# Optimization experiments

Measured on AMD Instinct MI355X. Metric: run time of the kernel, lower is better.

Reference implementation:

```python
import jax, jax.numpy as jnp
import numpy as np

N_NODES = 50000
N_EDGES = 800000
N_GRAPHS = 64
IN_C = 64
HID = 64
HEADS = 4
NEG_SLOPE = 0.2
EPS = 1e-16


def setup_inputs() -> dict:
    key = jax.random.key(0)
    ks = jax.random.split(key, 16)
    x = jax.random.normal(ks[0], (N_NODES, IN_C), dtype=jnp.float32)
    edge_index = jax.random.randint(ks[1], (2, N_EDGES), 0, N_NODES, dtype=jnp.int64)
    batch = jnp.sort(jax.random.randint(ks[2], (N_NODES,), 0, N_GRAPHS, dtype=jnp.int64))
    s = 1.0 / np.sqrt(IN_C)
    s2 = 1.0 / np.sqrt(HID * HEADS)
    s3 = 1.0 / np.sqrt(HID)
    return {
        "x": x,
        "edge_index": edge_index,
        "batch": batch,
        # GATv2 layer 1: in 64 -> heads*64 = 256 (concat)
        "Wl1": jax.random.normal(ks[3], (IN_C, HEADS * HID), dtype=jnp.float32) * s,
        "Wr1": jax.random.normal(ks[4], (IN_C, HEADS * HID), dtype=jnp.float32) * s,
        "att1": jax.random.normal(ks[5], (HEADS, HID), dtype=jnp.float32) * s3,
        "b1": jnp.zeros((HEADS * HID,), dtype=jnp.float32),
        # GATv2 layer 2: in 256 -> 1 head * 64
        "Wl2": jax.random.normal(ks[6], (HEADS * HID, HID), dtype=jnp.float32) * s2,
        "Wr2": jax.random.normal(ks[7], (HEADS * HID, HID), dtype=jnp.float32) * s2,
        "att2": jax.random.normal(ks[8], (1, HID), dtype=jnp.float32) * s3,
        "b2": jnp.zeros((HID,), dtype=jnp.float32),
        # MLP head: 64 -> 64 -> 2
        "W3": jax.random.normal(ks[9], (HID, 64), dtype=jnp.float32) * s3,
        "b3": jnp.zeros((64,), dtype=jnp.float32),
        "W4": jax.random.normal(ks[10], (64, 2), dtype=jnp.float32) * (1.0 / 8.0),
        "b4": jnp.zeros((2,), dtype=jnp.float32),
    }


def gatv2_conv(x, src, dst, Wl, Wr, att, bias, heads, out_c, n_nodes):
    # PyG GATv2Conv (eval mode, add_self_loops=False, concat heads):
    # x_l = lin_l(x) used for SOURCE nodes (messages), x_r = lin_r(x) for TARGET nodes.
    xl = (x @ Wl).reshape(n_nodes, heads, out_c)
    xr = (x @ Wr).reshape(n_nodes, heads, out_c)
    e = jax.nn.leaky_relu(xl[src] + xr[dst], NEG_SLOPE)          # [E, H, C]
    logits = jnp.einsum('ehc,hc->eh', e, att)                    # [E, H]
    # numerically stable softmax over incoming edges of each target node
    m = jax.ops.segment_max(logits, dst, num_segments=n_nodes)   # [N, H]
    ex = jnp.exp(logits - m[dst])
    denom = jax.ops.segment_sum(ex, dst, num_segments=n_nodes)   # [N, H]
    alpha = ex / (denom[dst] + EPS)                              # [E, H]
    out = jax.ops.segment_sum(alpha[:, :, None] * xl[src], dst, num_segments=n_nodes)
    return out.reshape(n_nodes, heads * out_c) + bias


def reference(x, edge_index, batch, Wl1, Wr1, att1, b1, Wl2, Wr2, att2, b2, W3, b3, W4, b4):
    src, dst = edge_index[0], edge_index[1]
    n = x.shape[0]
    h = gatv2_conv(x, src, dst, Wl1, Wr1, att1, b1, HEADS, HID, n)
    h = jax.nn.elu(h)
    h = gatv2_conv(h, src, dst, Wl2, Wr2, att2, b2, 1, HID, n)
    h = jax.nn.elu(h)
    # global mean pool over graphs
    sums = jax.ops.segment_sum(h, batch, num_segments=N_GRAPHS)
    cnt = jax.ops.segment_sum(jnp.ones((n,), dtype=h.dtype), batch, num_segments=N_GRAPHS)
    pooled = sums / jnp.maximum(cnt, 1.0)[:, None]
    # MLP head (dropout inactive in eval)
    z = jax.nn.relu(pooled @ W3 + b3)
    return z @ W4 + b4
```

## Files before the change

### kernel.cpp

```cpp
#include <hip/hip_runtime.h>
#include <hip/hip_fp16.h>
#include <math.h>

#define N_NODES 50000
#define N_EDGES 800000
#define N_GRAPHS 64
#define L2E 1.44269504f

#if __has_builtin(__builtin_amdgcn_fdot2)
#define HAS_FDOT2 1
typedef _Float16 h2_t __attribute__((ext_vector_type(2)));
#else
#define HAS_FDOT2 0
#endif

typedef _Float16 f16x8 __attribute__((ext_vector_type(8)));
typedef float f32x4 __attribute__((ext_vector_type(4)));

__device__ __forceinline__ float elu1(float v){ return v > 0.f ? v : expm1f(v); }

__device__ __forceinline__ __half2 bcast_h2(float e){
    return __builtin_bit_cast(__half2, __builtin_amdgcn_cvt_pkrtz(e, e));
}

__device__ __forceinline__ float pkdot(float4 q, const __half2* r2,
        const __half2* A6, const __half2* A4){
    const __half2* qh = (const __half2*)&q;
    float p = 0.f;
#if HAS_FDOT2
    #pragma unroll
    for (int i=0;i<4;i++){
        __half2 u = __hadd2(qh[i], r2[i]);
        __half2 ua = __builtin_bit_cast(__half2,
            __builtin_bit_cast(unsigned, u) & 0x7FFF7FFFu);
        p = __builtin_amdgcn_fdot2(__builtin_bit_cast(h2_t,u),
                                   __builtin_bit_cast(h2_t,A6[i]), p, false);
        p = __builtin_amdgcn_fdot2(__builtin_bit_cast(h2_t,ua),
                                   __builtin_bit_cast(h2_t,A4[i]), p, false);
    }
#else
    #pragma unroll
    for (int i=0;i<4;i++){
        float2 qf = __half22float2(qh[i]);
        float2 rf = __half22float2(r2[i]);
        float2 s6 = __half22float2(A6[i]);
        float2 s4 = __half22float2(A4[i]);
        float u0 = qf.x + rf.x, u1 = qf.y + rf.y;
        p = fmaf(s6.x, u0, fmaf(s4.x, fabsf(u0), p));
        p = fmaf(s6.y, u1, fmaf(s4.y, fabsf(u1), p));
    }
#endif
    return p;
}

__global__ __launch_bounds__(256) void k_prep(const float* __restrict__ x,
        const float* __restrict__ Wl1, const float* __restrict__ Wr1,
        const float* __restrict__ Wl2, const float* __restrict__ Wr2,
        const int* __restrict__ ei,
        __half* __restrict__ xh, __half* __restrict__ Wt1, __half* __restrict__ Wt2,
        int* __restrict__ deg, int* __restrict__ ranks, float* __restrict__ pooled){
    int t = threadIdx.x, bk = blockIdx.x;
    if (bk < 782){
        int e4 = bk*256 + t;
        if (e4 < N_EDGES/4){
            int4 d = ((const int4*)(ei + N_EDGES))[e4];
            int4 r;
            r.x = atomicAdd(&deg[d.x],1);
            r.y = atomicAdd(&deg[d.y],1);
            r.z = atomicAdd(&deg[d.z],1);
            r.w = atomicAdd(&deg[d.w],1);
            ((int4*)ranks)[e4] = r;
        }
    } else if (bk < 3907){
        int idx = (bk-782)*256 + t;
        float4 v = ((const float4*)x)[idx];
        __half2* dst = (__half2*)xh + (size_t)idx*2;
        dst[0] = __floats2half2_rn(v.x, v.y);
        dst[1] = __floats2half2_rn(v.z, v.w);
    } else {
        int elem = (bk-3907)*256 + t;
        if (elem < 32768){
            int c = elem >> 6, k = elem & 63;
            float v = (c < 256) ? Wl1[k*256 + c] : Wr1[k*256 + (c-256)];
            Wt1[elem] = __float2half(v);
        } else {
            int e2 = elem - 32768;
            int c = e2 >> 8, k = e2 & 255;
            float v = (c < 64) ? Wl2[k*64 + c] : Wr2[k*64 + (c-64)];
            Wt2[e2] = __float2half(v);
        }
        if (elem < N_GRAPHS*64) pooled[elem] = 0.f;
    }
}

__global__ __launch_bounds__(1024) void k_scan_a(const int* __restrict__ deg,
        int* __restrict__ rowptr, int* __restrict__ partial){
    __shared__ int s[1024];
    int t = threadIdx.x; int i = blockIdx.x*1024 + t;
    int v = (i < N_NODES) ? deg[i] : 0;
    s[t] = v; __syncthreads();
    for (int off=1; off<1024; off<<=1){
        int add = (t>=off) ? s[t-off] : 0;
        __syncthreads();
        s[t] += add;
        __syncthreads();
    }
    if (i < N_NODES) rowptr[i] = s[t] - v;
    if (t == 1023) partial[blockIdx.x] = s[1023];
}

__global__ __launch_bounds__(1024) void k_scan_c(int* __restrict__ rowptr,
        const int* __restrict__ partial){
    __shared__ int base;
    if (threadIdx.x == 0){
        int run = 0;
        for (int bk=0; bk<(int)blockIdx.x; bk++) run += partial[bk];
        base = run;
    }
    __syncthreads();
    int i = blockIdx.x*1024 + threadIdx.x;
    if (i < N_NODES){
        rowptr[i] += base;
    } else if (i == N_NODES){
        rowptr[N_NODES] = N_EDGES;
    }
}

__global__ __launch_bounds__(256) void k_mm1(const __half* __restrict__ xh,
        const __half* __restrict__ Wt1,
        __half* __restrict__ xl1h, __half* __restrict__ xr1h,
        const int* __restrict__ ei, const int* __restrict__ ranks,
        const int* __restrict__ rowptr, int* __restrict__ srcs){
    if (blockIdx.y == 0){
        int e4 = blockIdx.x*256 + threadIdx.x;
        if (e4 < N_EDGES/4){
            int4 sv = ((const int4*)ei)[e4];
            int4 dv = ((const int4*)(ei + N_EDGES))[e4];
            int4 rv = ((const int4*)ranks)[e4];
            __builtin_nontemporal_store(sv.x, &srcs[rowptr[dv.x] + rv.x]);
            __builtin_nontemporal_store(sv.y, &srcs[rowptr[dv.y] + rv.y]);
            __builtin_nontemporal_store(sv.z, &srcs[rowptr[dv.z] + rv.z]);
            __builtin_nontemporal_store(sv.w, &srcs[rowptr[dv.w] + rv.w]);
        }
        return;
    }
    __shared__ __half lds[4][16*136];
    int w = threadIdx.x >> 6, l = threadIdx.x & 63;
    int r0 = blockIdx.x*64 + w*16;
    int lr = l & 15, lk = l >> 4, lk4 = lk*4;
    int ar = r0 + lr; if (ar >= N_NODES) ar = N_NODES-1;
    const __half* arow = xh + (size_t)ar*64;
    f16x8 a0 = *(const f16x8*)(arow + lk*8);
    f16x8 a1 = *(const f16x8*)(arow + 32 + lk*8);
    #pragma unroll
    for (int cg=0; cg<4; cg++){
        f32x4 acc[8];
        #pragma unroll
        for (int ct=0; ct<8; ct++) acc[ct] = (f32x4){0.f,0.f,0.f,0.f};
        #pragma unroll
        for (int ct=0; ct<8; ct++){
            int col = cg*128 + ct*16 + lr;
            const __half* brow = Wt1 + (size_t)col*64;
            f16x8 b0 = *(const f16x8*)(brow + lk*8);
            f16x8 b1 = *(const f16x8*)(brow + 32 + lk*8);
            acc[ct] = __builtin_amdgcn_mfma_f32_16x16x32_f16(a0, b0, acc[ct], 0,0,0);
            acc[ct] = __builtin_amdgcn_mfma_f32_16x16x32_f16(a1, b1, acc[ct], 0,0,0);
        }
        #pragma unroll
        for (int ct=0; ct<8; ct++){
            #pragma unroll
            for (int i=0;i<4;i++)
                lds[w][(lk4+i)*136 + ct*16 + lr] = __float2half(acc[ct][i]);
        }
        __half* base = (cg < 2) ? xl1h : xr1h;
        int cbase = (cg & 1)*128;
        #pragma unroll
        for (int rr=0; rr<4; rr++){
            int row = rr*4 + lk;
            float4 v = *(const float4*)&lds[w][row*136 + lr*8];
            int grow = r0 + row;
            if (grow < N_NODES)
                *(float4*)&base[(size_t)grow*256 + cbase + lr*8] = v;
        }
    }
}

__global__ __launch_bounds__(256) void k_mm2(const __half* __restrict__ h1h,
        const __half* __restrict__ Wt2,
        __half* __restrict__ xl2h, __half* __restrict__ xr2h){
    __shared__ __half lds[4][16*72];
    int w = threadIdx.x >> 6, l = threadIdx.x & 63;
    int r0 = blockIdx.x*64 + w*16;
    int lr = l & 15, lk = l >> 4, lk4 = lk*4;
    int ar = r0 + lr; if (ar >= N_NODES) ar = N_NODES-1;
    const __half* arow = h1h + (size_t)ar*256;
    f16x8 a[8];
    #pragma unroll
    for (int ks=0; ks<8; ks++) a[ks] = *(const f16x8*)(arow + ks*32 + lk*8);
    #pragma unroll
    for (int cg=0; cg<2; cg++){
        f32x4 acc[4];
        #pragma unroll
        for (int ct=0; ct<4; ct++) acc[ct] = (f32x4){0.f,0.f,0.f,0.f};
        #pragma unroll
        for (int ks=0; ks<8; ks++){
            #pragma unroll
            for (int ct=0; ct<4; ct++){
                int col = cg*64 + ct*16 + lr;
                f16x8 bf = *(const f16x8*)(Wt2 + (size_t)col*256 + ks*32 + lk*8);
                acc[ct] = __builtin_amdgcn_mfma_f32_16x16x32_f16(a[ks], bf, acc[ct], 0,0,0);
            }
        }
        #pragma unroll
        for (int ct=0; ct<4; ct++){
            #pragma unroll
            for (int i=0;i<4;i++)
                lds[w][(lk4+i)*72 + ct*16 + lr] = __float2half(acc[ct][i]);
        }
        __half* base = (cg == 0) ? xl2h : xr2h;
        #pragma unroll
        for (int rr=0; rr<2; rr++){
            int row = rr*8 + (l>>3);
            float4 v = *(const float4*)&lds[w][row*72 + (l&7)*8];
            int grow = r0 + row;
            if (grow < N_NODES)
                *(float4*)&base[(size_t)grow*64 + (l&7)*8] = v;
        }
    }
}

__global__ __launch_bounds__(256) void k_gat1(const __half* __restrict__ xlh,
        const __half* __restrict__ xrh, const int* __restrict__ srcs,
        const int* __restrict__ rowptr, const float* __restrict__ att,
        const float* __restrict__ b, __half* __restrict__ h1h){
    int w = threadIdx.x >> 6, l = threadIdx.x & 63;
    int n = blockIdx.x*4 + w;
    int g = l >> 5, sub = l & 31;
    const float4* xh4 = (const float4*)xlh;
    float4 rq = *(const float4*)(xrh + (size_t)n*256 + sub*8);
    __half2 r2[4];
    { const __half2* rh = (const __half2*)&rq;
      r2[0]=rh[0]; r2[1]=rh[1]; r2[2]=rh[2]; r2[3]=rh[3]; }
    float4 A0v = *(const float4*)(att + sub*8);
    float4 A1v = *(const float4*)(att + sub*8 + 4);
    const float C6 = 0.6f*L2E, C4 = 0.4f*L2E;
    __half2 A6[4] = { __floats2half2_rn(A0v.x*C6, A0v.y*C6),
                      __floats2half2_rn(A0v.z*C6, A0v.w*C6),
                      __floats2half2_rn(A1v.x*C6, A1v.y*C6),
                      __floats2half2_rn(A1v.z*C6, A1v.w*C6) };
    __half2 A4[4] = { __floats2half2_rn(A0v.x*C4, A0v.y*C4),
                      __floats2half2_rn(A0v.z*C4, A0v.w*C4),
                      __floats2half2_rn(A1v.x*C4, A1v.y*C4),
                      __floats2half2_rn(A1v.z*C4, A1v.w*C4) };
    const __half2 Z2 = __floats2half2_rn(0.f, 0.f);
    float accf[8];
    #pragma unroll
    for (int c=0;c<8;c++) accf[c]=0.f;
    float dacc = 0.f;
    int beg = rowptr[n], end = rowptr[n+1];

    auto body = [&](int j, bool checked){
        int j0=j+g, j1=j+2+g, j2=j+4+g, j3=j+6+g;
        bool c0=true, c1=true, c2=true, c3=true;
        if (checked){
            c0 = j0<end; c1 = j1<end; c2 = j2<end; c3 = j3<end;
            j0 = c0?j0:beg; j1 = c1?j1:beg; j2 = c2?j2:beg; j3 = c3?j3:beg;
        }
        int s0 = srcs[j0], s1 = srcs[j1], s2 = srcs[j2], s3 = srcs[j3];
        float4 q0 = xh4[(unsigned)(s0*32 + sub)];
        float4 q1 = xh4[(unsigned)(s1*32 + sub)];
        float4 q2 = xh4[(unsigned)(s2*32 + sub)];
        float4 q3 = xh4[(unsigned)(s3*32 + sub)];
        float p0 = pkdot(q0, r2, A6, A4);
        float p1 = pkdot(q1, r2, A6, A4);
        float p2 = pkdot(q2, r2, A6, A4);
        float p3 = pkdot(q3, r2, A6, A4);
        #pragma unroll
        for (int off=1; off<8; off<<=1){
            p0 += __shfl_xor(p0, off);
            p1 += __shfl_xor(p1, off);
            p2 += __shfl_xor(p2, off);
            p3 += __shfl_xor(p3, off);
        }
        float e0 = exp2f(p0), e1 = exp2f(p1), e2 = exp2f(p2), e3 = exp2f(p3);
        if (checked){
            e0 = c0?e0:0.f; e1 = c1?e1:0.f; e2 = c2?e2:0.f; e3 = c3?e3:0.f;
        }
        __half2 E0 = bcast_h2(e0);
        __half2 E1 = bcast_h2(e1);
        __half2 E2 = bcast_h2(e2);
        __half2 E3 = bcast_h2(e3);
        const __half2* q0h = (const __half2*)&q0;
        const __half2* q1h = (const __half2*)&q1;
        const __half2* q2h = (const __half2*)&q2;
        const __half2* q3h = (const __half2*)&q3;
        #pragma unroll
        for (int i=0;i<4;i++){
            __half2 a16 = __hfma2(E0, q0h[i], Z2);
            a16 = __hfma2(E1, q1h[i], a16);
            a16 = __hfma2(E2, q2h[i], a16);
            a16 = __hfma2(E3, q3h[i], a16);
            float2 f = __half22float2(a16);
            accf[2*i]   += f.x;
            accf[2*i+1] += f.y;
        }
        dacc += e0 + e1 + e2 + e3;
    };

    int j = beg;
    int nfull = (end - beg) >> 3;
    for (int it=0; it<nfull; ++it, j+=8) body(j, false);
    if (j < end) body(j, true);

    #pragma unroll
    for (int c=0;c<8;c++) accf[c] += __shfl_xor(accf[c], 32);
    dacc += __shfl_xor(dacc, 32);
    if (l < 32){
        float inv = 1.f / (dacc + 1e-16f);
        float4 B0 = *(const float4*)(b + l*8);
        float4 B1 = *(const float4*)(b + l*8 + 4);
        float4 st;
        __half2* sp = (__half2*)&st;
        sp[0] = __floats2half2_rn(elu1(fmaf(accf[0],inv,B0.x)), elu1(fmaf(accf[1],inv,B0.y)));
        sp[1] = __floats2half2_rn(elu1(fmaf(accf[2],inv,B0.z)), elu1(fmaf(accf[3],inv,B0.w)));
        sp[2] = __floats2half2_rn(elu1(fmaf(accf[4],inv,B1.x)), elu1(fmaf(accf[5],inv,B1.y)));
        sp[3] = __floats2half2_rn(elu1(fmaf(accf[6],inv,B1.z)), elu1(fmaf(accf[7],inv,B1.w)));
        *(float4*)(h1h + (size_t)n*256 + l*8) = st;
    }
}

__global__ __launch_bounds__(256) void k_gat2(const __half* __restrict__ xlh,
        const __half* __restrict__ xrh, const int* __restrict__ srcs,
        const int* __restrict__ rowptr, const float* __restrict__ att,
        const float* __restrict__ b, float* __restrict__ h2){
    int w = threadIdx.x >> 6, l = threadIdx.x & 63;
    int n = blockIdx.x*4 + w;
    int g = l >> 3, sub = l & 7;
    const float4* xh4 = (const float4*)xlh;
    float4 rq = *(const float4*)(xrh + (size_t)n*64 + sub*8);
    __half2 r2[4];
    { const __half2* rh = (const __half2*)&rq;
      r2[0]=rh[0]; r2[1]=rh[1]; r2[2]=rh[2]; r2[3]=rh[3]; }
    float4 A0v = *(const float4*)(att + sub*8);
    float4 A1v = *(const float4*)(att + sub*8 + 4);
    const float C6 = 0.6f*L2E, C4 = 0.4f*L2E;
    __half2 A6[4] = { __floats2half2_rn(A0v.x*C6, A0v.y*C6),
                      __floats2half2_rn(A0v.z*C6, A0v.w*C6),
                      __floats2half2_rn(A1v.x*C6, A1v.y*C6),
                      __floats2half2_rn(A1v.z*C6, A1v.w*C6) };
    __half2 A4[4] = { __floats2half2_rn(A0v.x*C4, A0v.y*C4),
                      __floats2half2_rn(A0v.z*C4, A0v.w*C4),
                      __floats2half2_rn(A1v.x*C4, A1v.y*C4),
                      __floats2half2_rn(A1v.z*C4, A1v.w*C4) };
    const __half2 Z2 = __floats2half2_rn(0.f, 0.f);
    __half2 a16[4] = {Z2, Z2, Z2, Z2};
    float dacc = 0.f;
    int beg = rowptr[n], end = rowptr[n+1];

    auto body = [&](int j, bool checked){
        int j0 = j+g, j1 = j+8+g;
        bool c0=true, c1=true;
        if (checked){
            c0 = j0<end; c1 = j1<end;
            j0 = c0?j0:beg; j1 = c1?j1:beg;
        }
        int s0 = srcs[j0], s1 = srcs[j1];
        float4 q0 = xh4[(unsigned)(s0*8 + sub)];
        float4 q1 = xh4[(unsigned)(s1*8 + sub)];
        float p0 = pkdot(q0, r2, A6, A4);
        float p1 = pkdot(q1, r2, A6, A4);
        #pragma unroll
        for (int off=1; off<8; off<<=1){
            p0 += __shfl_xor(p0, off);
            p1 += __shfl_xor(p1, off);
        }
        float e0 = exp2f(p0), e1 = exp2f(p1);
        if (checked){ e0 = c0?e0:0.f; e1 = c1?e1:0.f; }
        __half2 E0 = bcast_h2(e0);
        __half2 E1 = bcast_h2(e1);
        const __half2* q0h = (const __half2*)&q0;
        const __half2* q1h = (const __half2*)&q1;
        #pragma unroll
        for (int i=0;i<4;i++){
            a16[i] = __hfma2(E0, q0h[i], a16[i]);
            a16[i] = __hfma2(E1, q1h[i], a16[i]);
        }
        dacc += e0 + e1;
    };

    int j = beg;
    int nfull = (end - beg) >> 4;
    for (int it=0; it<nfull; ++it, j+=16) body(j, false);
    if (j < end) body(j, true);

    float accf[8];
    #pragma unroll
    for (int i=0;i<4;i++){
        float2 f = __half22float2(a16[i]);
        accf[2*i] = f.x; accf[2*i+1] = f.y;
    }
    #pragma unroll
    for (int off=8; off<64; off<<=1){
        #pragma unroll
        for (int c=0;c<8;c++) accf[c] += __shfl_xor(accf[c], off);
        dacc += __shfl_xor(dacc, off);
    }
    if (l < 8){
        float inv = 1.f / (dacc + 1e-16f);
        float4 B0 = *(const float4*)(b + l*8);
        float4 B1 = *(const float4*)(b + l*8 + 4);
        float4 o0, o1;
        o0.x = elu1(fmaf(accf[0], inv, B0.x));
        o0.y = elu1(fmaf(accf[1], inv, B0.y));
        o0.z = elu1(fmaf(accf[2], inv, B0.z));
        o0.w = elu1(fmaf(accf[3], inv, B0.w));
        o1.x = elu1(fmaf(accf[4], inv, B1.x));
        o1.y = elu1(fmaf(accf[5], inv, B1.y));
        o1.z = elu1(fmaf(accf[6], inv, B1.z));
        o1.w = elu1(fmaf(accf[7], inv, B1.w));
        float4* op = (float4*)(h2 + (size_t)n*64 + l*8);
        op[0] = o0; op[1] = o1;
    }
}

__device__ __forceinline__ int lower_bound_i(const int* a, int n, int key){
    int lo = 0, hi = n;
    while (lo < hi){ int mid = (lo+hi)>>1; if (a[mid] < key) lo = mid+1; else hi = mid; }
    return lo;
}

__global__ __launch_bounds__(256) void k_pool(const float* __restrict__ h2,
        const int* __restrict__ batch, float* __restrict__ pooled){
    int gph = blockIdx.x, part = blockIdx.y;
    int t = threadIdx.x, c = t & 63, q = t >> 6;
    int start = lower_bound_i(batch, N_NODES, gph);
    int end   = lower_bound_i(batch, N_NODES, gph+1);
    int len = end - start;
    int is = start + (int)(((long long)len*part) >> 3);
    int ie = start + (int)(((long long)len*(part+1)) >> 3);
    float s = 0.f;
    for (int i = is + q; i < ie; i += 4) s += h2[(size_t)i*64 + c];
    __shared__ float red[256];
    red[t] = s; __syncthreads();
    if (q == 0){
        float tot = red[c] + red[64+c] + red[128+c] + red[192+c];
        atomicAdd(&pooled[gph*64 + c], tot);
    }
}

__global__ __launch_bounds__(64) void k_mlp(const float* __restrict__ pooled,
        const int* __restrict__ batch,
        const float* __restrict__ W3, const float* __restrict__ b3,
        const float* __restrict__ W4, const float* __restrict__ b4,
        float* __restrict__ out){
    int gph = blockIdx.x, t = threadIdx.x;
    __shared__ float ps[64], zs[64];
    int start = lower_bound_i(batch, N_NODES, gph);
    int end   = lower_bound_i(batch, N_NODES, gph+1);
    float cnt = fmaxf((float)(end - start), 1.f);
    ps[t] = pooled[gph*64 + t] / cnt;
    __syncthreads();
    float a = b3[t];
    for (int k=0;k<64;k++) a = fmaf(ps[k], W3[k*64+t], a);
    zs[t] = fmaxf(a, 0.f); __syncthreads();
    if (t < 2){
        float o = b4[t];
        for (int k=0;k<64;k++) o = fmaf(zs[k], W4[k*2+t], o);
        out[gph*2 + t] = o;
    }
}

extern "C" void kernel_launch(void* const* d_in, const int* in_sizes, int n_in,
                              void* d_out, int out_size, void* d_ws, size_t ws_size,
                              hipStream_t stream) {
    const float* x    = (const float*)d_in[0];
    const int*   ei   = (const int*)  d_in[1];
    const int*   batch= (const int*)  d_in[2];
    const float* Wl1  = (const float*)d_in[3];
    const float* Wr1  = (const float*)d_in[4];
    const float* att1 = (const float*)d_in[5];
    const float* b1   = (const float*)d_in[6];
    const float* Wl2  = (const float*)d_in[7];
    const float* Wr2  = (const float*)d_in[8];
    const float* att2 = (const float*)d_in[9];
    const float* b2   = (const float*)d_in[10];
    const float* W3   = (const float*)d_in[11];
    const float* b3   = (const float*)d_in[12];
    const float* W4   = (const float*)d_in[13];
    const float* b4   = (const float*)d_in[14];
    float* out = (float*)d_out;

    char* wsp = (char*)d_ws;
    size_t off = 0;
    auto alloc = [&](size_t bytes) -> char* {
        char* p = wsp + off; off += (bytes + 255) & ~(size_t)255; return p;
    };
    __half* xh    = (__half*)alloc((size_t)N_NODES*64*2);
    __half* Wt1   = (__half*)alloc(512*64*2);
    __half* Wt2   = (__half*)alloc(128*256*2);
    __half* xl1h  = (__half*)alloc((size_t)N_NODES*256*2);
    __half* xr1h  = (__half*)alloc((size_t)N_NODES*256*2);
    __half* h1h   = (__half*)alloc((size_t)N_NODES*256*2);
    int* rowptr   = (int*)alloc((N_NODES+1)*4);
    int* partial  = (int*)alloc(64*4);
    int* srcs     = (int*)alloc((size_t)N_EDGES*4);
    int* ranks    = (int*)alloc((size_t)N_EDGES*4);
    int* deg      = (int*)alloc(N_NODES*4);
    float* pooled = (float*)alloc(N_GRAPHS*64*4);
    __half* xl2h  = xl1h;
    __half* xr2h  = xl1h + (size_t)N_NODES*64;
    float*  h2    = (float*)xr1h;

    hipMemsetAsync(deg, 0, (size_t)N_NODES*sizeof(int), stream);
    k_prep<<<782+3125+256, 256, 0, stream>>>(x, Wl1, Wr1, Wl2, Wr2, ei,
                                             xh, Wt1, Wt2, deg, ranks, pooled);
    k_scan_a<<<49, 1024, 0, stream>>>(deg, rowptr, partial);
    k_scan_c<<<49, 1024, 0, stream>>>(rowptr, partial);

    k_mm1<<<dim3(782,2), 256, 0, stream>>>(xh, Wt1, xl1h, xr1h,
                                           ei, ranks, rowptr, srcs);
    k_gat1<<<N_NODES/4, 256, 0, stream>>>(xl1h, xr1h, srcs, rowptr, att1, b1, h1h);
    k_mm2<<<782, 256, 0, stream>>>(h1h, Wt2, xl2h, xr2h);
    k_gat2<<<N_NODES/4, 256, 0, stream>>>(xl2h, xr2h, srcs, rowptr, att2, b2, h2);
    k_pool<<<dim3(N_GRAPHS,8), 256, 0, stream>>>(h2, batch, pooled);
    k_mlp<<<N_GRAPHS, 64, 0, stream>>>(pooled, batch, W3, b3, W4, b4, out);
}
```

Before: 263.9 us.

## Privatize degree counters into 8 partitions and store layer-2 output in fp16

The degree-counting atomics are spread across 8 per-partition copies chosen by block index, which is meant to cut atomic contention on hot destination nodes. The scan then combines the partitions into per-partition offsets, and the CSR fill adds that offset using a partition tag packed into the high bits of each rank. The layer-2 GAT output is now written as fp16 and the pool kernel reads half2 values, which halves that traffic at some cost in precision. This also adds a larger memset, an extra offsets array and an extra gather in the fill.

```diff
diff --git a/kernel.cpp b/kernel.cpp
--- a/kernel.cpp
+++ b/kernel.cpp
@@ -6,6 +6,8 @@
 #define N_EDGES 800000
 #define N_GRAPHS 64
 #define L2E 1.44269504f
+#define NPAD 50176
+#define NPART 8
 
 #if __has_builtin(__builtin_amdgcn_fdot2)
 #define HAS_FDOT2 1
@@ -58,17 +60,20 @@
         const float* __restrict__ Wl2, const float* __restrict__ Wr2,
         const int* __restrict__ ei,
         __half* __restrict__ xh, __half* __restrict__ Wt1, __half* __restrict__ Wt2,
-        int* __restrict__ deg, int* __restrict__ ranks, float* __restrict__ pooled){
+        int* __restrict__ deg8, int* __restrict__ ranks, float* __restrict__ pooled){
     int t = threadIdx.x, bk = blockIdx.x;
     if (bk < 782){
         int e4 = bk*256 + t;
         if (e4 < N_EDGES/4){
+            int part = bk & (NPART-1);
+            int* dp = deg8 + part*NPAD;
+            int ptag = part << 27;
             int4 d = ((const int4*)(ei + N_EDGES))[e4];
             int4 r;
-            r.x = atomicAdd(&deg[d.x],1);
-            r.y = atomicAdd(&deg[d.y],1);
-            r.z = atomicAdd(&deg[d.z],1);
-            r.w = atomicAdd(&deg[d.w],1);
+            r.x = atomicAdd(&dp[d.x],1) | ptag;
+            r.y = atomicAdd(&dp[d.y],1) | ptag;
+            r.z = atomicAdd(&dp[d.z],1) | ptag;
+            r.w = atomicAdd(&dp[d.w],1) | ptag;
             ((int4*)ranks)[e4] = r;
         }
     } else if (bk < 3907){
@@ -93,11 +98,20 @@
     }
 }
 
-__global__ __launch_bounds__(1024) void k_scan_a(const int* __restrict__ deg,
-        int* __restrict__ rowptr, int* __restrict__ partial){
+__global__ __launch_bounds__(1024) void k_scan_a(const int* __restrict__ deg8,
+        int* __restrict__ off8, int* __restrict__ rowptr, int* __restrict__ partial){
     __shared__ int s[1024];
     int t = threadIdx.x; int i = blockIdx.x*1024 + t;
-    int v = (i < N_NODES) ? deg[i] : 0;
+    int v = 0;
+    if (i < N_NODES){
+        int run = 0;
+        #pragma unroll
+        for (int xp=0; xp<NPART; xp++){
+            off8[xp*NPAD + i] = run;
+            run += deg8[xp*NPAD + i];
+        }
+        v = run;
+    }
     s[t] = v; __syncthreads();
     for (int off=1; off<1024; off<<=1){
         int add = (t>=off) ? s[t-off] : 0;
@@ -130,17 +144,22 @@
         const __half* __restrict__ Wt1,
         __half* __restrict__ xl1h, __half* __restrict__ xr1h,
         const int* __restrict__ ei, const int* __restrict__ ranks,
-        const int* __restrict__ rowptr, int* __restrict__ srcs){
+        const int* __restrict__ rowptr, const int* __restrict__ off8,
+        int* __restrict__ srcs){
     if (blockIdx.y == 0){
         int e4 = blockIdx.x*256 + threadIdx.x;
         if (e4 < N_EDGES/4){
             int4 sv = ((const int4*)ei)[e4];
             int4 dv = ((const int4*)(ei + N_EDGES))[e4];
             int4 rv = ((const int4*)ranks)[e4];
-            __builtin_nontemporal_store(sv.x, &srcs[rowptr[dv.x] + rv.x]);
-            __builtin_nontemporal_store(sv.y, &srcs[rowptr[dv.y] + rv.y]);
-            __builtin_nontemporal_store(sv.z, &srcs[rowptr[dv.z] + rv.z]);
-            __builtin_nontemporal_store(sv.w, &srcs[rowptr[dv.w] + rv.w]);
+            int p0 = (unsigned)rv.x >> 27, r0 = rv.x & 0x07FFFFFF;
+            int p1 = (unsigned)rv.y >> 27, r1 = rv.y & 0x07FFFFFF;
+            int p2 = (unsigned)rv.z >> 27, r2 = rv.z & 0x07FFFFFF;
+            int p3 = (unsigned)rv.w >> 27, r3 = rv.w & 0x07FFFFFF;
+            __builtin_nontemporal_store(sv.x, &srcs[rowptr[dv.x] + off8[p0*NPAD + dv.x] + r0]);
+            __builtin_nontemporal_store(sv.y, &srcs[rowptr[dv.y] + off8[p1*NPAD + dv.y] + r1]);
+            __builtin_nontemporal_store(sv.z, &srcs[rowptr[dv.z] + off8[p2*NPAD + dv.z] + r2]);
+            __builtin_nontemporal_store(sv.w, &srcs[rowptr[dv.w] + off8[p3*NPAD + dv.w] + r3]);
         }
         return;
     }
@@ -332,7 +351,7 @@
 __global__ __launch_bounds__(256) void k_gat2(const __half* __restrict__ xlh,
         const __half* __restrict__ xrh, const int* __restrict__ srcs,
         const int* __restrict__ rowptr, const float* __restrict__ att,
-        const float* __restrict__ b, float* __restrict__ h2){
+        const float* __restrict__ b, __half* __restrict__ h2h){
     int w = threadIdx.x >> 6, l = threadIdx.x & 63;
     int n = blockIdx.x*4 + w;
     int g = l >> 3, sub = l & 7;
@@ -409,17 +428,13 @@
         float inv = 1.f / (dacc + 1e-16f);
         float4 B0 = *(const float4*)(b + l*8);
         float4 B1 = *(const float4*)(b + l*8 + 4);
-        float4 o0, o1;
-        o0.x = elu1(fmaf(accf[0], inv, B0.x));
-        o0.y = elu1(fmaf(accf[1], inv, B0.y));
-        o0.z = elu1(fmaf(accf[2], inv, B0.z));
-        o0.w = elu1(fmaf(accf[3], inv, B0.w));
-        o1.x = elu1(fmaf(accf[4], inv, B1.x));
-        o1.y = elu1(fmaf(accf[5], inv, B1.y));
-        o1.z = elu1(fmaf(accf[6], inv, B1.z));
-        o1.w = elu1(fmaf(accf[7], inv, B1.w));
-        float4* op = (float4*)(h2 + (size_t)n*64 + l*8);
-        op[0] = o0; op[1] = o1;
+        float4 st;
+        __half2* sp = (__half2*)&st;
+        sp[0] = __floats2half2_rn(elu1(fmaf(accf[0],inv,B0.x)), elu1(fmaf(accf[1],inv,B0.y)));
+        sp[1] = __floats2half2_rn(elu1(fmaf(accf[2],inv,B0.z)), elu1(fmaf(accf[3],inv,B0.w)));
+        sp[2] = __floats2half2_rn(elu1(fmaf(accf[4],inv,B1.x)), elu1(fmaf(accf[5],inv,B1.y)));
+        sp[3] = __floats2half2_rn(elu1(fmaf(accf[6],inv,B1.z)), elu1(fmaf(accf[7],inv,B1.w)));
+        *(float4*)(h2h + (size_t)n*64 + l*8) = st;
     }
 }
 
@@ -429,22 +444,32 @@
     return lo;
 }
 
-__global__ __launch_bounds__(256) void k_pool(const float* __restrict__ h2,
+__global__ __launch_bounds__(256) void k_pool(const __half* __restrict__ h2h,
         const int* __restrict__ batch, float* __restrict__ pooled){
     int gph = blockIdx.x, part = blockIdx.y;
-    int t = threadIdx.x, c = t & 63, q = t >> 6;
+    int t = threadIdx.x, c2 = t & 31, q = t >> 5;
     int start = lower_bound_i(batch, N_NODES, gph);
     int end   = lower_bound_i(batch, N_NODES, gph+1);
     int len = end - start;
     int is = start + (int)(((long long)len*part) >> 3);
     int ie = start + (int)(((long long)len*(part+1)) >> 3);
-    float s = 0.f;
-    for (int i = is + q; i < ie; i += 4) s += h2[(size_t)i*64 + c];
-    __shared__ float red[256];
+    float2 s = make_float2(0.f, 0.f);
+    const __half2* h22 = (const __half2*)h2h;
+    for (int i = is + q; i < ie; i += 8){
+        float2 f = __half22float2(h22[(unsigned)(i*32 + c2)]);
+        s.x += f.x; s.y += f.y;
+    }
+    __shared__ float2 red[256];
     red[t] = s; __syncthreads();
     if (q == 0){
-        float tot = red[c] + red[64+c] + red[128+c] + red[192+c];
-        atomicAdd(&pooled[gph*64 + c], tot);
+        float2 tot = red[c2];
+        #pragma unroll
+        for (int qq=1; qq<8; qq++){
+            tot.x += red[qq*32 + c2].x;
+            tot.y += red[qq*32 + c2].y;
+        }
+        atomicAdd(&pooled[gph*64 + c2*2],     tot.x);
+        atomicAdd(&pooled[gph*64 + c2*2 + 1], tot.y);
     }
 }
 
@@ -505,23 +530,24 @@
     int* partial  = (int*)alloc(64*4);
     int* srcs     = (int*)alloc((size_t)N_EDGES*4);
     int* ranks    = (int*)alloc((size_t)N_EDGES*4);
-    int* deg      = (int*)alloc(N_NODES*4);
+    int* deg8     = (int*)alloc((size_t)NPART*NPAD*4);
+    int* off8     = (int*)alloc((size_t)NPART*NPAD*4);
     float* pooled = (float*)alloc(N_GRAPHS*64*4);
     __half* xl2h  = xl1h;
     __half* xr2h  = xl1h + (size_t)N_NODES*64;
-    float*  h2    = (float*)xr1h;
-
-    hipMemsetAsync(deg, 0, (size_t)N_NODES*sizeof(int), stream);
+    __half* h2h   = (__half*)xr1h;
+
+    hipMemsetAsync(deg8, 0, (size_t)NPART*NPAD*sizeof(int), stream);
     k_prep<<<782+3125+256, 256, 0, stream>>>(x, Wl1, Wr1, Wl2, Wr2, ei,
-                                             xh, Wt1, Wt2, deg, ranks, pooled);
-    k_scan_a<<<49, 1024, 0, stream>>>(deg, rowptr, partial);
+                                             xh, Wt1, Wt2, deg8, ranks, pooled);
+    k_scan_a<<<49, 1024, 0, stream>>>(deg8, off8, rowptr, partial);
     k_scan_c<<<49, 1024, 0, stream>>>(rowptr, partial);
 
     k_mm1<<<dim3(782,2), 256, 0, stream>>>(xh, Wt1, xl1h, xr1h,
-                                           ei, ranks, rowptr, srcs);
+                                           ei, ranks, rowptr, off8, srcs);
     k_gat1<<<N_NODES/4, 256, 0, stream>>>(xl1h, xr1h, srcs, rowptr, att1, b1, h1h);
     k_mm2<<<782, 256, 0, stream>>>(h1h, Wt2, xl2h, xr2h);
-    k_gat2<<<N_NODES/4, 256, 0, stream>>>(xl2h, xr2h, srcs, rowptr, att2, b2, h2);
-    k_pool<<<dim3(N_GRAPHS,8), 256, 0, stream>>>(h2, batch, pooled);
+    k_gat2<<<N_NODES/4, 256, 0, stream>>>(xl2h, xr2h, srcs, rowptr, att2, b2, h2h);
+    k_pool<<<dim3(N_GRAPHS,8), 256, 0, stream>>>(h2h, batch, pooled);
     k_mlp<<<N_GRAPHS, 64, 0, stream>>>(pooled, batch, W3, b3, W4, b4, out);
 }
```

Result: no change. 259.4 us (-1.7%).
